# Performance work log

Hardware: AMD Instinct MI355X
Metric: run time of the kernel (lower is better)

Reference implementation:

```python
import jax, jax.numpy as jnp
import numpy as np

L, B, S, D, H, FF = 6, 6, 7, 512, 8, 2048  # layers, support-set size+1, nodes(1 verb + 6 nouns), dim, heads, ffn
HD = D // H


def setup_inputs() -> dict:
    key = jax.random.key(0)
    ks = jax.random.split(key, 16)
    n = lambda k, shape: jax.random.normal(k, shape, dtype=jnp.float32) * 0.02
    z = lambda shape: jnp.zeros(shape, jnp.float32)
    o = lambda shape: jnp.ones(shape, jnp.float32)
    return {
        'features': jax.random.normal(ks[0], (B, S, D), dtype=jnp.float32),
        'role_tokens': jax.random.normal(ks[1], (B, S - 1, D), dtype=jnp.float32),
        'in_w': n(ks[2], (L, 3 * D, D)), 'in_b': z((L, 3 * D)),
        'out_w': n(ks[3], (L, D, D)), 'out_b': z((L, D)),
        'ln1_w': o((L, D)), 'ln1_b': z((L, D)),
        'ln2_w': o((L, D)), 'ln2_b': z((L, D)),
        'ln3_w': o((L, D)), 'ln3_b': z((L, D)),
        'ln4_w': o((L, D)), 'ln4_b': z((L, D)),
        'f1_w1': n(ks[4], (L, FF, D)), 'f1_b1': z((L, FF)),
        'f1_w2': n(ks[5], (L, D, FF)), 'f1_b2': z((L, D)),
        'f2_w1': n(ks[6], (L, FF, D)), 'f2_b1': z((L, FF)),
        'f2_w2': n(ks[7], (L, D, FF)), 'f2_b2': z((L, D)),
        'a1_w': n(ks[8], (L, D, D * 5)), 'a1_b': z((L, D)),
        'a2_w': n(ks[9], (L, D, D * 6)), 'a2_b': z((L, D)),
    }


def _ln(x, w, b):
    mu = jnp.mean(x, -1, keepdims=True)
    var = jnp.mean(jnp.square(x - mu), -1, keepdims=True)
    return (x - mu) * jax.lax.rsqrt(var + 1e-5) * w + b


def _forward(features, role_tokens, in_w, in_b, out_w, out_b, ln1_w, ln1_b, ln2_w, ln2_b,
             ln3_w, ln3_b, ln4_w, ln4_b, f1_w1, f1_b1, f1_w2, f1_b2, f2_w1, f2_b1,
             f2_w2, f2_b2, a1_w, a1_b, a2_w, a2_b):
    def step(x, p):
        (iw, ib, ow, ob, l1w, l1b, l2w, l2b, l3w, l3b, l4w, l4b,
         w11, b11, w12, b12, w21, b21, w22, b22, aw1, ab1, aw2, ab2) = p
        # batched tiny self-attention over the 7 nodes of each of the 6 support examples
        src = x.at[:, 1:, :].add(role_tokens)                      # role embed on noun slots only
        qkv = jnp.einsum('bsd,ed->bse', src, iw) + ib              # (B,S,3D)
        q, k, v = jnp.split(qkv, 3, axis=-1)
        q = q.reshape(B, S, H, HD); k = k.reshape(B, S, H, HD); v = v.reshape(B, S, H, HD)
        att = jax.nn.softmax(jnp.einsum('bqhd,bkhd->bhqk', q, k) / jnp.sqrt(jnp.float32(HD)), axis=-1)
        ctx = jnp.einsum('bhqk,bkhd->bqhd', att, v).reshape(B, S, D)
        msg = jnp.einsum('bsd,ed->bse', ctx, ow) + ob              # (B,S,D)
        verb_msg = msg[:, 0, :]                                    # (B,D)
        noun_msg = msg[:, 1:, :]                                   # (B,S-1,D)
        # gated concat-aggregation
        agg_verb = jax.nn.sigmoid(verb_msg[1:].reshape(-1) @ aw1.T + ab1)  # (D,) from 5 support verb msgs
        agg_noun = jax.nn.sigmoid(noun_msg[0].reshape(-1) @ aw2.T + ab2)   # (D,) from 6 target noun msgs
        # noun update for target example (index 0)
        s = _ln(x[0, 1:, :] + agg_verb, l1w, l1b)                  # (6,D)
        s = _ln(s + (jax.nn.relu(s @ w11.T + b11) @ w12.T + b12), l2w, l2b)
        # verb update for target example
        t = _ln(x[0, 0, :] + agg_noun, l3w, l3b)                   # (D,)
        t = _ln(t + (jax.nn.relu(t @ w21.T + b21) @ w22.T + b22), l4w, l4b)
        new_self = jnp.concatenate([t[None, :], s], axis=0)        # (S,D)
        return jnp.concatenate([new_self[None], x[1:]], axis=0), None

    params = (in_w, in_b, out_w, out_b, ln1_w, ln1_b, ln2_w, ln2_b, ln3_w, ln3_b,
              ln4_w, ln4_b, f1_w1, f1_b1, f1_w2, f1_b2, f2_w1, f2_b1, f2_w2, f2_b2,
              a1_w, a1_b, a2_w, a2_b)
    out, _ = jax.lax.scan(step, features, params)
    return out[0:1]                                                # (1,7,512)


def reference(features, role_tokens, in_w, in_b, out_w, out_b, ln1_w, ln1_b, ln2_w, ln2_b,
              ln3_w, ln3_b, ln4_w, ln4_b, f1_w1, f1_b1, f1_w2, f1_b2, f2_w1, f2_b1,
              f2_w2, f2_b2, a1_w, a1_b, a2_w, a2_b):
    return _forward(features, role_tokens, in_w, in_b, out_w, out_b, ln1_w, ln1_b,
                    ln2_w, ln2_b, ln3_w, ln3_b, ln4_w, ln4_b, f1_w1, f1_b1, f1_w2, f1_b2,
                    f2_w1, f2_b1, f2_w2, f2_b2, a1_w, a1_b, a2_w, a2_b)
```

## Files before the change

kernel.cpp:

```cpp
#include <hip/hip_runtime.h>
#include <math.h>

#define NL 6
#define NB 6
#define NS 7
#define ND 512
#define NH 8
#define HDIM 64
#define NFF 2048
#define NROWS (NB*NS)

__device__ __forceinline__ float wave_sum(float v) {
    v += __shfl_down(v, 32, 64);
    v += __shfl_down(v, 16, 64);
    v += __shfl_down(v, 8, 64);
    v += __shfl_down(v, 4, 64);
    v += __shfl_down(v, 2, 64);
    v += __shfl_down(v, 1, 64);
    return v;
}

__device__ __forceinline__ float dot512(const float* __restrict__ a,
                                        const float* __restrict__ b, int lane) {
    int d0 = lane * 8;
    float4 a1 = *(const float4*)(a + d0);
    float4 a2 = *(const float4*)(a + d0 + 4);
    float4 b1 = *(const float4*)(b + d0);
    float4 b2 = *(const float4*)(b + d0 + 4);
    return a1.x*b1.x + a1.y*b1.y + a1.z*b1.z + a1.w*b1.w
         + a2.x*b2.x + a2.y*b2.y + a2.z*b2.z + a2.w*b2.w;
}

__global__ void qkv_kernel(const float* __restrict__ features,
                           const float* __restrict__ role,
                           const float* __restrict__ cur,
                           const float* __restrict__ iw,
                           const float* __restrict__ ib,
                           float* __restrict__ qkv) {
    int gw = (blockIdx.x * blockDim.x + threadIdx.x) >> 6;
    int lane = threadIdx.x & 63;
    if (gw >= NROWS * 1536) return;
    int row = gw / 1536;
    int e = gw - row * 1536;
    int b = row / NS, s = row - b * NS;
    const float* src = (b == 0) ? (cur + s * ND) : (features + row * ND);
    int d0 = lane * 8;
    float4 s1 = *(const float4*)(src + d0);
    float4 s2 = *(const float4*)(src + d0 + 4);
    if (s > 0) {
        const float* rp = role + (b * (NS-1) + (s-1)) * ND + d0;
        float4 r1 = *(const float4*)(rp);
        float4 r2 = *(const float4*)(rp + 4);
        s1.x += r1.x; s1.y += r1.y; s1.z += r1.z; s1.w += r1.w;
        s2.x += r2.x; s2.y += r2.y; s2.z += r2.z; s2.w += r2.w;
    }
    const float* wr = iw + e * ND + d0;
    float4 w1 = *(const float4*)(wr);
    float4 w2 = *(const float4*)(wr + 4);
    float acc = s1.x*w1.x + s1.y*w1.y + s1.z*w1.z + s1.w*w1.w
              + s2.x*w2.x + s2.y*w2.y + s2.z*w2.z + s2.w*w2.w;
    acc = wave_sum(acc);
    if (lane == 0) qkv[row * 1536 + e] = acc + ib[e];
}

__global__ void attn_kernel(const float* __restrict__ qkv, float* __restrict__ ctx) {
    int b = blockIdx.x >> 3, h = blockIdx.x & 7;
    int lane = threadIdx.x;
    __shared__ float q[NS][HDIM], k[NS][HDIM], v[NS][HDIM], att[NS][NS];
    for (int s = 0; s < NS; s++) {
        const float* base = qkv + (size_t)(b*NS + s) * 1536 + h * HDIM + lane;
        q[s][lane] = base[0];
        k[s][lane] = base[ND];
        v[s][lane] = base[2*ND];
    }
    __syncthreads();
    if (lane < NS*NS) {
        int i = lane / NS, j = lane - (lane / NS) * NS;
        float acc = 0.f;
        for (int d = 0; d < HDIM; d++) acc += q[i][d] * k[j][d];
        att[i][j] = acc * 0.125f;
    }
    __syncthreads();
    if (lane < NS) {
        float m = -1e30f;
        for (int j = 0; j < NS; j++) m = fmaxf(m, att[lane][j]);
        float e[NS]; float sum = 0.f;
        for (int j = 0; j < NS; j++) { e[j] = expf(att[lane][j] - m); sum += e[j]; }
        float inv = 1.f / sum;
        for (int j = 0; j < NS; j++) att[lane][j] = e[j] * inv;
    }
    __syncthreads();
    for (int s = 0; s < NS; s++) {
        float acc = 0.f;
        for (int j = 0; j < NS; j++) acc += att[s][j] * v[j][lane];
        ctx[(size_t)(b*NS + s) * ND + h * HDIM + lane] = acc;
    }
}

__global__ void msg_kernel(const float* __restrict__ ctx,
                           const float* __restrict__ ow,
                           const float* __restrict__ ob,
                           float* __restrict__ msg) {
    int gw = (blockIdx.x * blockDim.x + threadIdx.x) >> 6;
    int lane = threadIdx.x & 63;
    if (gw >= NROWS * ND) return;
    int row = gw / ND, e = gw - row * ND;
    float acc = wave_sum(dot512(ctx + (size_t)row * ND, ow + (size_t)e * ND, lane));
    if (lane == 0) msg[row * ND + e] = acc + ob[e];
}

__global__ void agg_kernel(const float* __restrict__ msg,
                           const float* __restrict__ aw1, const float* __restrict__ ab1,
                           const float* __restrict__ aw2, const float* __restrict__ ab2,
                           float* __restrict__ aggv, float* __restrict__ aggn) {
    int gw = (blockIdx.x * blockDim.x + threadIdx.x) >> 6;
    int lane = threadIdx.x & 63;
    if (gw < ND) {
        int j = gw;
        float acc = 0.f;
        for (int c = 0; c < 5; c++)
            acc += dot512(msg + (size_t)(c+1)*NS*ND, aw1 + (size_t)j*2560 + c*ND, lane);
        acc = wave_sum(acc);
        if (lane == 0) aggv[j] = 1.f / (1.f + expf(-(acc + ab1[j])));
    } else if (gw < 2*ND) {
        int j = gw - ND;
        float acc = 0.f;
        for (int c = 0; c < 6; c++)
            acc += dot512(msg + (size_t)(c+1)*ND, aw2 + (size_t)j*3072 + c*ND, lane);
        acc = wave_sum(acc);
        if (lane == 0) aggn[j] = 1.f / (1.f + expf(-(acc + ab2[j])));
    }
}

__global__ void ln13_kernel(const float* __restrict__ cur,
                            const float* __restrict__ aggv, const float* __restrict__ aggn,
                            const float* __restrict__ l1w, const float* __restrict__ l1b,
                            const float* __restrict__ l3w, const float* __restrict__ l3b,
                            float* __restrict__ xln) {
    int r = blockIdx.x, t = threadIdx.x;
    const float* agg = (r == 0) ? aggn : aggv;
    const float* w   = (r == 0) ? l3w : l1w;
    const float* bb  = (r == 0) ? l3b : l1b;
    float x0 = cur[r*ND + t]       + agg[t];
    float x1 = cur[r*ND + 256 + t] + agg[256 + t];
    __shared__ float sd[4];
    int lane = t & 63, wv = t >> 6;
    float v = wave_sum(x0 + x1);
    if (lane == 0) sd[wv] = v;
    __syncthreads();
    float mu = (sd[0] + sd[1] + sd[2] + sd[3]) * (1.f / ND);
    __syncthreads();
    float d0 = x0 - mu, d1 = x1 - mu;
    v = wave_sum(d0*d0 + d1*d1);
    if (lane == 0) sd[wv] = v;
    __syncthreads();
    float var = (sd[0] + sd[1] + sd[2] + sd[3]) * (1.f / ND);
    float inv = rsqrtf(var + 1e-5f);
    xln[r*ND + t]       = d0 * inv * w[t]     + bb[t];
    xln[r*ND + 256 + t] = d1 * inv * w[256+t] + bb[256+t];
}

__global__ void ffa_kernel(const float* __restrict__ xln,
                           const float* __restrict__ w11, const float* __restrict__ b11,
                           const float* __restrict__ w21, const float* __restrict__ b21,
                           float* __restrict__ h) {
    int gw = (blockIdx.x * blockDim.x + threadIdx.x) >> 6;
    int lane = threadIdx.x & 63;
    if (gw >= NS * NFF) return;
    int r = gw / NFF, f = gw - r * NFF;
    const float* W = (r == 0) ? (w21 + (size_t)f * ND) : (w11 + (size_t)f * ND);
    const float* bias = (r == 0) ? b21 : b11;
    float acc = wave_sum(dot512(xln + r * ND, W, lane));
    if (lane == 0) h[r * NFF + f] = fmaxf(acc + bias[f], 0.f);
}

__global__ void ffb_kernel(const float* __restrict__ xln, const float* __restrict__ hbuf,
                           const float* __restrict__ w12, const float* __restrict__ b12,
                           const float* __restrict__ w22, const float* __restrict__ b22,
                           float* __restrict__ ff) {
    int gw = (blockIdx.x * blockDim.x + threadIdx.x) >> 6;
    int lane = threadIdx.x & 63;
    if (gw >= NS * ND) return;
    int r = gw / ND, d = gw - r * ND;
    const float* W = (r == 0) ? (w22 + (size_t)d * NFF) : (w12 + (size_t)d * NFF);
    const float* bias = (r == 0) ? b22 : b12;
    const float* hin = hbuf + r * NFF;
    float acc = 0.f;
    for (int c = 0; c < 4; c++) acc += dot512(hin + c*ND, W + c*ND, lane);
    acc = wave_sum(acc);
    if (lane == 0) ff[r * ND + d] = xln[r * ND + d] + acc + bias[d];
}

__global__ void ln24_kernel(const float* __restrict__ ff,
                            const float* __restrict__ l2w, const float* __restrict__ l2b,
                            const float* __restrict__ l4w, const float* __restrict__ l4b,
                            float* __restrict__ cur, float* __restrict__ outp) {
    int r = blockIdx.x, t = threadIdx.x;
    const float* w  = (r == 0) ? l4w : l2w;
    const float* bb = (r == 0) ? l4b : l2b;
    float x0 = ff[r*ND + t], x1 = ff[r*ND + 256 + t];
    __shared__ float sd[4];
    int lane = t & 63, wv = t >> 6;
    float v = wave_sum(x0 + x1);
    if (lane == 0) sd[wv] = v;
    __syncthreads();
    float mu = (sd[0] + sd[1] + sd[2] + sd[3]) * (1.f / ND);
    __syncthreads();
    float d0 = x0 - mu, d1 = x1 - mu;
    v = wave_sum(d0*d0 + d1*d1);
    if (lane == 0) sd[wv] = v;
    __syncthreads();
    float var = (sd[0] + sd[1] + sd[2] + sd[3]) * (1.f / ND);
    float inv = rsqrtf(var + 1e-5f);
    float y0 = d0 * inv * w[t]     + bb[t];
    float y1 = d1 * inv * w[256+t] + bb[256+t];
    cur[r*ND + t]       = y0;
    cur[r*ND + 256 + t] = y1;
    if (outp) {
        outp[r*ND + t]       = y0;
        outp[r*ND + 256 + t] = y1;
    }
}

extern "C" void kernel_launch(void* const* d_in, const int* in_sizes, int n_in,
                              void* d_out, int out_size, void* d_ws, size_t ws_size,
                              hipStream_t stream) {
    const float* features = (const float*)d_in[0];
    const float* role     = (const float*)d_in[1];
    const float* in_w  = (const float*)d_in[2];
    const float* in_b  = (const float*)d_in[3];
    const float* out_w = (const float*)d_in[4];
    const float* out_b = (const float*)d_in[5];
    const float* ln1_w = (const float*)d_in[6];
    const float* ln1_b = (const float*)d_in[7];
    const float* ln2_w = (const float*)d_in[8];
    const float* ln2_b = (const float*)d_in[9];
    const float* ln3_w = (const float*)d_in[10];
    const float* ln3_b = (const float*)d_in[11];
    const float* ln4_w = (const float*)d_in[12];
    const float* ln4_b = (const float*)d_in[13];
    const float* f1_w1 = (const float*)d_in[14];
    const float* f1_b1 = (const float*)d_in[15];
    const float* f1_w2 = (const float*)d_in[16];
    const float* f1_b2 = (const float*)d_in[17];
    const float* f2_w1 = (const float*)d_in[18];
    const float* f2_b1 = (const float*)d_in[19];
    const float* f2_w2 = (const float*)d_in[20];
    const float* f2_b2 = (const float*)d_in[21];
    const float* a1_w  = (const float*)d_in[22];
    const float* a1_b  = (const float*)d_in[23];
    const float* a2_w  = (const float*)d_in[24];
    const float* a2_b  = (const float*)d_in[25];

    float* ws   = (float*)d_ws;
    float* cur  = ws;
    float* qkv  = ws + 3584;
    float* ctx  = qkv + 64512;
    float* msg  = ctx + 21504;
    float* aggv = msg + 21504;
    float* aggn = aggv + 512;
    float* xln  = aggn + 512;
    float* hbuf = xln + 3584;
    float* ff   = hbuf + 14336;

    hipMemcpyAsync(cur, features, 3584 * sizeof(float), hipMemcpyDeviceToDevice, stream);

    for (int l = 0; l < NL; l++) {
        qkv_kernel<<<NROWS*1536/4, 256, 0, stream>>>(
            features, role, cur, in_w + (size_t)l*1536*ND, in_b + (size_t)l*1536, qkv);
        attn_kernel<<<NB*NH, 64, 0, stream>>>(qkv, ctx);
        msg_kernel<<<NROWS*ND/4, 256, 0, stream>>>(
            ctx, out_w + (size_t)l*ND*ND, out_b + (size_t)l*ND, msg);
        agg_kernel<<<2*ND/4, 256, 0, stream>>>(
            msg, a1_w + (size_t)l*ND*2560, a1_b + (size_t)l*ND,
                 a2_w + (size_t)l*ND*3072, a2_b + (size_t)l*ND, aggv, aggn);
        ln13_kernel<<<NS, 256, 0, stream>>>(
            cur, aggv, aggn, ln1_w + (size_t)l*ND, ln1_b + (size_t)l*ND,
            ln3_w + (size_t)l*ND, ln3_b + (size_t)l*ND, xln);
        ffa_kernel<<<NS*NFF/4, 256, 0, stream>>>(
            xln, f1_w1 + (size_t)l*NFF*ND, f1_b1 + (size_t)l*NFF,
                 f2_w1 + (size_t)l*NFF*ND, f2_b1 + (size_t)l*NFF, hbuf);
        ffb_kernel<<<NS*ND/4, 256, 0, stream>>>(
            xln, hbuf, f1_w2 + (size_t)l*ND*NFF, f1_b2 + (size_t)l*ND,
                       f2_w2 + (size_t)l*ND*NFF, f2_b2 + (size_t)l*ND, ff);
        ln24_kernel<<<NS, 256, 0, stream>>>(
            ff, ln2_w + (size_t)l*ND, ln2_b + (size_t)l*ND,
                ln4_w + (size_t)l*ND, ln4_b + (size_t)l*ND,
            cur, (l == NL-1) ? (float*)d_out : nullptr);
    }
}
```

Measured before the change: 474.8 us.

## Replace per-layer kernel chain with single persistent kernel and grid barriers

Replaces the eight kernels launched per layer with one persistent 256-block kernel that uses software grid barriers built on atomics. Because only example 0 depends on the previous layer, the support-example K/V projections, their attention, out-projection and aggregation are precomputed for all layers up front. The serial per-layer path then handles only the target example. The change also fuses the layer norms into neighbouring stages and reuses register-held weights across several rows. It removes launch overhead and redundant per-layer work, at the cost of relying on all blocks being co-resident for the spin barriers and of extra workspace.

```diff
diff --git a/kernel.cpp b/kernel.cpp
--- a/kernel.cpp
+++ b/kernel.cpp
@@ -2,13 +2,8 @@
 #include <math.h>
 
 #define NL 6
-#define NB 6
-#define NS 7
 #define ND 512
-#define NH 8
-#define HDIM 64
 #define NFF 2048
-#define NROWS (NB*NS)
 
 __device__ __forceinline__ float wave_sum(float v) {
     v += __shfl_down(v, 32, 64);
@@ -19,9 +14,25 @@
     v += __shfl_down(v, 1, 64);
     return v;
 }
-
-__device__ __forceinline__ float dot512(const float* __restrict__ a,
-                                        const float* __restrict__ b, int lane) {
+__device__ __forceinline__ float wave_sum_all(float v) {
+    v += __shfl_xor(v, 32, 64);
+    v += __shfl_xor(v, 16, 64);
+    v += __shfl_xor(v, 8, 64);
+    v += __shfl_xor(v, 4, 64);
+    v += __shfl_xor(v, 2, 64);
+    v += __shfl_xor(v, 1, 64);
+    return v;
+}
+
+__device__ __forceinline__ float dot8(const float* a, int lane, float4 w1, float4 w2) {
+    int d0 = lane * 8;
+    float4 x1 = *(const float4*)(a + d0);
+    float4 x2 = *(const float4*)(a + d0 + 4);
+    return x1.x*w1.x + x1.y*w1.y + x1.z*w1.z + x1.w*w1.w
+         + x2.x*w2.x + x2.y*w2.y + x2.z*w2.z + x2.w*w2.w;
+}
+__device__ __forceinline__ float dotg(const float* __restrict__ a,
+                                      const float* __restrict__ b, int lane) {
     int d0 = lane * 8;
     float4 a1 = *(const float4*)(a + d0);
     float4 a2 = *(const float4*)(a + d0 + 4);
@@ -31,194 +42,366 @@
          + a2.x*b2.x + a2.y*b2.y + a2.z*b2.z + a2.w*b2.w;
 }
 
-__global__ void qkv_kernel(const float* __restrict__ features,
-                           const float* __restrict__ role,
-                           const float* __restrict__ cur,
-                           const float* __restrict__ iw,
-                           const float* __restrict__ ib,
-                           float* __restrict__ qkv) {
-    int gw = (blockIdx.x * blockDim.x + threadIdx.x) >> 6;
-    int lane = threadIdx.x & 63;
-    if (gw >= NROWS * 1536) return;
-    int row = gw / 1536;
-    int e = gw - row * 1536;
-    int b = row / NS, s = row - b * NS;
-    const float* src = (b == 0) ? (cur + s * ND) : (features + row * ND);
-    int d0 = lane * 8;
-    float4 s1 = *(const float4*)(src + d0);
-    float4 s2 = *(const float4*)(src + d0 + 4);
-    if (s > 0) {
-        const float* rp = role + (b * (NS-1) + (s-1)) * ND + d0;
-        float4 r1 = *(const float4*)(rp);
-        float4 r2 = *(const float4*)(rp + 4);
-        s1.x += r1.x; s1.y += r1.y; s1.z += r1.z; s1.w += r1.w;
-        s2.x += r2.x; s2.y += r2.y; s2.z += r2.z; s2.w += r2.w;
-    }
-    const float* wr = iw + e * ND + d0;
-    float4 w1 = *(const float4*)(wr);
-    float4 w2 = *(const float4*)(wr + 4);
-    float acc = s1.x*w1.x + s1.y*w1.y + s1.z*w1.z + s1.w*w1.w
-              + s2.x*w2.x + s2.y*w2.y + s2.z*w2.z + s2.w*w2.w;
-    acc = wave_sum(acc);
-    if (lane == 0) qkv[row * 1536 + e] = acc + ib[e];
-}
-
-__global__ void attn_kernel(const float* __restrict__ qkv, float* __restrict__ ctx) {
-    int b = blockIdx.x >> 3, h = blockIdx.x & 7;
-    int lane = threadIdx.x;
-    __shared__ float q[NS][HDIM], k[NS][HDIM], v[NS][HDIM], att[NS][NS];
-    for (int s = 0; s < NS; s++) {
-        const float* base = qkv + (size_t)(b*NS + s) * 1536 + h * HDIM + lane;
-        q[s][lane] = base[0];
-        k[s][lane] = base[ND];
-        v[s][lane] = base[2*ND];
-    }
+__device__ __forceinline__ void stats8(float4 f1, float4 f2, float& mu, float& inv) {
+    float s = f1.x+f1.y+f1.z+f1.w + f2.x+f2.y+f2.z+f2.w;
+    s = wave_sum_all(s);
+    mu = s * (1.f/512.f);
+    float q = (f1.x-mu)*(f1.x-mu) + (f1.y-mu)*(f1.y-mu) + (f1.z-mu)*(f1.z-mu) + (f1.w-mu)*(f1.w-mu)
+            + (f2.x-mu)*(f2.x-mu) + (f2.y-mu)*(f2.y-mu) + (f2.z-mu)*(f2.z-mu) + (f2.w-mu)*(f2.w-mu);
+    q = wave_sum_all(q);
+    inv = rsqrtf(q * (1.f/512.f) + 1e-5f);
+}
+__device__ __forceinline__ void ln_apply(float4& f1, float4& f2, float mu, float inv,
+                                         const float* __restrict__ w,
+                                         const float* __restrict__ b, int d0) {
+    float4 w1 = *(const float4*)(w + d0), w2 = *(const float4*)(w + d0 + 4);
+    float4 b1 = *(const float4*)(b + d0), b2 = *(const float4*)(b + d0 + 4);
+    f1.x = (f1.x-mu)*inv*w1.x + b1.x; f1.y = (f1.y-mu)*inv*w1.y + b1.y;
+    f1.z = (f1.z-mu)*inv*w1.z + b1.z; f1.w = (f1.w-mu)*inv*w1.w + b1.w;
+    f2.x = (f2.x-mu)*inv*w2.x + b2.x; f2.y = (f2.y-mu)*inv*w2.y + b2.y;
+    f2.z = (f2.z-mu)*inv*w2.z + b2.z; f2.w = (f2.w-mu)*inv*w2.w + b2.w;
+}
+
+__device__ __forceinline__ void gbar(unsigned* bar, int k) {
+    __threadfence();
     __syncthreads();
-    if (lane < NS*NS) {
-        int i = lane / NS, j = lane - (lane / NS) * NS;
-        float acc = 0.f;
-        for (int d = 0; d < HDIM; d++) acc += q[i][d] * k[j][d];
-        att[i][j] = acc * 0.125f;
+    if (threadIdx.x == 0) {
+        int sub = blockIdx.x & 7;
+        unsigned v = __hip_atomic_fetch_add(&bar[sub*16], 1u, __ATOMIC_RELAXED, __HIP_MEMORY_SCOPE_AGENT);
+        if (v == 32u*(unsigned)(k+1) - 1u) {
+            unsigned tt = __hip_atomic_fetch_add(&bar[128], 1u, __ATOMIC_RELAXED, __HIP_MEMORY_SCOPE_AGENT);
+            if (tt == 8u*(unsigned)(k+1) - 1u)
+                __hip_atomic_fetch_add(&bar[144], 1u, __ATOMIC_RELEASE, __HIP_MEMORY_SCOPE_AGENT);
+        }
+        while (__hip_atomic_load(&bar[144], __ATOMIC_RELAXED, __HIP_MEMORY_SCOPE_AGENT) < (unsigned)(k+1))
+            __builtin_amdgcn_s_sleep(4);
     }
     __syncthreads();
-    if (lane < NS) {
-        float m = -1e30f;
-        for (int j = 0; j < NS; j++) m = fmaxf(m, att[lane][j]);
-        float e[NS]; float sum = 0.f;
-        for (int j = 0; j < NS; j++) { e[j] = expf(att[lane][j] - m); sum += e[j]; }
-        float inv = 1.f / sum;
-        for (int j = 0; j < NS; j++) att[lane][j] = e[j] * inv;
+    __threadfence();
+}
+
+__global__ __launch_bounds__(256, 2)
+void fused_persistent(const float* __restrict__ features, const float* __restrict__ role,
+                      const float* __restrict__ in_w,  const float* __restrict__ in_b,
+                      const float* __restrict__ out_w, const float* __restrict__ out_b,
+                      const float* __restrict__ ln1_w, const float* __restrict__ ln1_b,
+                      const float* __restrict__ ln2_w, const float* __restrict__ ln2_b,
+                      const float* __restrict__ ln3_w, const float* __restrict__ ln3_b,
+                      const float* __restrict__ ln4_w, const float* __restrict__ ln4_b,
+                      const float* __restrict__ f1_w1, const float* __restrict__ f1_b1,
+                      const float* __restrict__ f1_w2, const float* __restrict__ f1_b2,
+                      const float* __restrict__ f2_w1, const float* __restrict__ f2_b1,
+                      const float* __restrict__ f2_w2, const float* __restrict__ f2_b2,
+                      const float* __restrict__ a1_w,  const float* __restrict__ a1_b,
+                      const float* __restrict__ a2_w,  const float* __restrict__ a2_b,
+                      unsigned* bar, float* wsf, float* __restrict__ outp)
+{
+    __shared__ float lds[18432];
+    __shared__ float sred[16];
+    const int t = threadIdx.x, bid = blockIdx.x;
+    const int wv = t >> 6, lane = t & 63;
+    const int gw = bid * 4 + wv;
+    const int d0 = lane * 8;
+    int bk = 0;
+
+    float* qkv_pre  = wsf;
+    float* msg_pre  = qkv_pre + 322560;
+    float* aggv_pre = msg_pre + 15360;
+    float* qkv0     = aggv_pre + 3072;
+    float* msg0     = qkv0 + 10752;
+    float* aggn     = msg0 + 3072;
+    float* hbuf     = aggn + 512;
+    float* xlnws    = hbuf + 14336;
+    float* ffA      = xlnws + 3584;
+    float* ffB      = ffA + 3584;
+
+    for (int i = t; i < 35*ND; i += 256) {
+        int m = i >> 9, d = i & 511;
+        int b = m / 7 + 1, s = m - (m/7)*7;
+        float v = features[(b*7+s)*ND + d];
+        if (s > 0) v += role[(b*6 + s-1)*ND + d];
+        lds[i] = v;
     }
     __syncthreads();
-    for (int s = 0; s < NS; s++) {
-        float acc = 0.f;
-        for (int j = 0; j < NS; j++) acc += att[s][j] * v[j][lane];
-        ctx[(size_t)(b*NS + s) * ND + h * HDIM + lane] = acc;
-    }
-}
-
-__global__ void msg_kernel(const float* __restrict__ ctx,
-                           const float* __restrict__ ow,
-                           const float* __restrict__ ob,
-                           float* __restrict__ msg) {
-    int gw = (blockIdx.x * blockDim.x + threadIdx.x) >> 6;
-    int lane = threadIdx.x & 63;
-    if (gw >= NROWS * ND) return;
-    int row = gw / ND, e = gw - row * ND;
-    float acc = wave_sum(dot512(ctx + (size_t)row * ND, ow + (size_t)e * ND, lane));
-    if (lane == 0) msg[row * ND + e] = acc + ob[e];
-}
-
-__global__ void agg_kernel(const float* __restrict__ msg,
-                           const float* __restrict__ aw1, const float* __restrict__ ab1,
-                           const float* __restrict__ aw2, const float* __restrict__ ab2,
-                           float* __restrict__ aggv, float* __restrict__ aggn) {
-    int gw = (blockIdx.x * blockDim.x + threadIdx.x) >> 6;
-    int lane = threadIdx.x & 63;
-    if (gw < ND) {
-        int j = gw;
-        float acc = 0.f;
+    for (int k = 0; k < 9; k++) {
+        int p = gw + (k << 10);
+        int l, e; bool kv;
+        if (p < 6144) { l = p >> 10; e = 512 + (p & 1023); kv = true; }
+        else { int q = p - 6144; l = q >> 9; e = q & 511; kv = false; }
+        const float* wr = in_w + ((size_t)l*1536 + e)*ND + d0;
+        float4 w1 = *(const float4*)wr, w2 = *(const float4*)(wr + 4);
+        float bias = in_b[l*1536 + e];
+        if (kv) {
+            for (int m = 0; m < 35; m++) {
+                float a = dot8(&lds[m*ND], lane, w1, w2);
+                a = wave_sum(a);
+                if (lane == 0) qkv_pre[((size_t)l*35 + m)*1536 + e] = a + bias;
+            }
+        } else {
+            for (int bb = 0; bb < 5; bb++) {
+                int m = bb * 7;
+                float a = dot8(&lds[m*ND], lane, w1, w2);
+                a = wave_sum(a);
+                if (lane == 0) qkv_pre[((size_t)l*35 + m)*1536 + e] = a + bias;
+            }
+        }
+    }
+    gbar(bar, bk++);
+
+    if (bid < 240) {
+        int g = bid >> 3, sub = bid & 7;
+        int l = g / 5, b = g - l*5 + 1;
+        float* kl = lds;
+        float* vl = lds + 3584;
+        float* ql = lds + 7168;
+        float* cl = lds + 7680;
+        float* at = lds + 8192;
+        size_t base = ((size_t)l*35 + (b-1)*7) * 1536;
+        for (int i = t; i < 3584; i += 256) {
+            int s = i >> 9, d = i & 511;
+            kl[i] = qkv_pre[base + (size_t)s*1536 + 512 + d];
+            vl[i] = qkv_pre[base + (size_t)s*1536 + 1024 + d];
+        }
+        for (int i = t; i < 512; i += 256) ql[i] = qkv_pre[base + i];
+        __syncthreads();
+        if (t < 56) {
+            int h = t / 7, kk = t - (t/7)*7;
+            float a = 0.f;
+            for (int d = 0; d < 64; d++) a += ql[h*64 + d] * kl[kk*512 + h*64 + d];
+            at[t] = a * 0.125f;
+        }
+        __syncthreads();
+        if (t < 8) {
+            float m = -1e30f;
+            for (int j = 0; j < 7; j++) m = fmaxf(m, at[t*7 + j]);
+            float e[7], ss = 0.f;
+            for (int j = 0; j < 7; j++) { e[j] = expf(at[t*7 + j] - m); ss += e[j]; }
+            float inv = 1.f / ss;
+            for (int j = 0; j < 7; j++) at[t*7 + j] = e[j] * inv;
+        }
+        __syncthreads();
+        for (int i = t; i < 512; i += 256) {
+            int h = i >> 6;
+            float a = 0.f;
+            for (int kk = 0; kk < 7; kk++) a += at[h*7 + kk] * vl[kk*512 + i];
+            cl[i] = a;
+        }
+        __syncthreads();
+        for (int i = 0; i < 16; i++) {
+            int e = sub*64 + wv*16 + i;
+            const float* wr = out_w + ((size_t)l*512 + e)*ND + d0;
+            float4 w1 = *(const float4*)wr, w2 = *(const float4*)(wr + 4);
+            float a = dot8(cl, lane, w1, w2);
+            a = wave_sum(a);
+            if (lane == 0) msg_pre[((size_t)l*5 + b-1)*512 + e] = a + out_b[l*512 + e];
+        }
+    }
+    gbar(bar, bk++);
+
+    for (int k = 0; k < 3; k++) {
+        int p = gw + (k << 10);
+        int l = p >> 9, j = p & 511;
+        const float* wj = a1_w + (size_t)l*1310720 + (size_t)j*2560;
+        float a = 0.f;
         for (int c = 0; c < 5; c++)
-            acc += dot512(msg + (size_t)(c+1)*NS*ND, aw1 + (size_t)j*2560 + c*ND, lane);
-        acc = wave_sum(acc);
-        if (lane == 0) aggv[j] = 1.f / (1.f + expf(-(acc + ab1[j])));
-    } else if (gw < 2*ND) {
-        int j = gw - ND;
-        float acc = 0.f;
-        for (int c = 0; c < 6; c++)
-            acc += dot512(msg + (size_t)(c+1)*ND, aw2 + (size_t)j*3072 + c*ND, lane);
-        acc = wave_sum(acc);
-        if (lane == 0) aggn[j] = 1.f / (1.f + expf(-(acc + ab2[j])));
-    }
-}
-
-__global__ void ln13_kernel(const float* __restrict__ cur,
-                            const float* __restrict__ aggv, const float* __restrict__ aggn,
-                            const float* __restrict__ l1w, const float* __restrict__ l1b,
-                            const float* __restrict__ l3w, const float* __restrict__ l3b,
-                            float* __restrict__ xln) {
-    int r = blockIdx.x, t = threadIdx.x;
-    const float* agg = (r == 0) ? aggn : aggv;
-    const float* w   = (r == 0) ? l3w : l1w;
-    const float* bb  = (r == 0) ? l3b : l1b;
-    float x0 = cur[r*ND + t]       + agg[t];
-    float x1 = cur[r*ND + 256 + t] + agg[256 + t];
-    __shared__ float sd[4];
-    int lane = t & 63, wv = t >> 6;
-    float v = wave_sum(x0 + x1);
-    if (lane == 0) sd[wv] = v;
-    __syncthreads();
-    float mu = (sd[0] + sd[1] + sd[2] + sd[3]) * (1.f / ND);
-    __syncthreads();
-    float d0 = x0 - mu, d1 = x1 - mu;
-    v = wave_sum(d0*d0 + d1*d1);
-    if (lane == 0) sd[wv] = v;
-    __syncthreads();
-    float var = (sd[0] + sd[1] + sd[2] + sd[3]) * (1.f / ND);
-    float inv = rsqrtf(var + 1e-5f);
-    xln[r*ND + t]       = d0 * inv * w[t]     + bb[t];
-    xln[r*ND + 256 + t] = d1 * inv * w[256+t] + bb[256+t];
-}
-
-__global__ void ffa_kernel(const float* __restrict__ xln,
-                           const float* __restrict__ w11, const float* __restrict__ b11,
-                           const float* __restrict__ w21, const float* __restrict__ b21,
-                           float* __restrict__ h) {
-    int gw = (blockIdx.x * blockDim.x + threadIdx.x) >> 6;
-    int lane = threadIdx.x & 63;
-    if (gw >= NS * NFF) return;
-    int r = gw / NFF, f = gw - r * NFF;
-    const float* W = (r == 0) ? (w21 + (size_t)f * ND) : (w11 + (size_t)f * ND);
-    const float* bias = (r == 0) ? b21 : b11;
-    float acc = wave_sum(dot512(xln + r * ND, W, lane));
-    if (lane == 0) h[r * NFF + f] = fmaxf(acc + bias[f], 0.f);
-}
-
-__global__ void ffb_kernel(const float* __restrict__ xln, const float* __restrict__ hbuf,
-                           const float* __restrict__ w12, const float* __restrict__ b12,
-                           const float* __restrict__ w22, const float* __restrict__ b22,
-                           float* __restrict__ ff) {
-    int gw = (blockIdx.x * blockDim.x + threadIdx.x) >> 6;
-    int lane = threadIdx.x & 63;
-    if (gw >= NS * ND) return;
-    int r = gw / ND, d = gw - r * ND;
-    const float* W = (r == 0) ? (w22 + (size_t)d * NFF) : (w12 + (size_t)d * NFF);
-    const float* bias = (r == 0) ? b22 : b12;
-    const float* hin = hbuf + r * NFF;
-    float acc = 0.f;
-    for (int c = 0; c < 4; c++) acc += dot512(hin + c*ND, W + c*ND, lane);
-    acc = wave_sum(acc);
-    if (lane == 0) ff[r * ND + d] = xln[r * ND + d] + acc + bias[d];
-}
-
-__global__ void ln24_kernel(const float* __restrict__ ff,
-                            const float* __restrict__ l2w, const float* __restrict__ l2b,
-                            const float* __restrict__ l4w, const float* __restrict__ l4b,
-                            float* __restrict__ cur, float* __restrict__ outp) {
-    int r = blockIdx.x, t = threadIdx.x;
-    const float* w  = (r == 0) ? l4w : l2w;
-    const float* bb = (r == 0) ? l4b : l2b;
-    float x0 = ff[r*ND + t], x1 = ff[r*ND + 256 + t];
-    __shared__ float sd[4];
-    int lane = t & 63, wv = t >> 6;
-    float v = wave_sum(x0 + x1);
-    if (lane == 0) sd[wv] = v;
-    __syncthreads();
-    float mu = (sd[0] + sd[1] + sd[2] + sd[3]) * (1.f / ND);
-    __syncthreads();
-    float d0 = x0 - mu, d1 = x1 - mu;
-    v = wave_sum(d0*d0 + d1*d1);
-    if (lane == 0) sd[wv] = v;
-    __syncthreads();
-    float var = (sd[0] + sd[1] + sd[2] + sd[3]) * (1.f / ND);
-    float inv = rsqrtf(var + 1e-5f);
-    float y0 = d0 * inv * w[t]     + bb[t];
-    float y1 = d1 * inv * w[256+t] + bb[256+t];
-    cur[r*ND + t]       = y0;
-    cur[r*ND + 256 + t] = y1;
-    if (outp) {
-        outp[r*ND + t]       = y0;
-        outp[r*ND + 256 + t] = y1;
+            a += dotg(msg_pre + ((size_t)l*5 + c)*512, wj + c*512, lane);
+        a = wave_sum(a);
+        if (lane == 0) aggv_pre[l*512 + j] = 1.f / (1.f + expf(-(a + a1_b[l*512 + j])));
+    }
+    gbar(bar, bk++);
+
+    const float* ffprev = nullptr;
+    #pragma unroll 1
+    for (int l = 0; l < NL; l++) {
+        float* ffcur = (l & 1) ? ffB : ffA;
+
+        for (int rr = wv; rr < 7; rr += 4) {
+            float4 f1, f2;
+            if (l == 0) {
+                const float* sp = features + rr*ND + d0;
+                f1 = *(const float4*)sp; f2 = *(const float4*)(sp + 4);
+            } else {
+                const float* sp = ffprev + rr*ND + d0;
+                f1 = *(const float4*)sp; f2 = *(const float4*)(sp + 4);
+                float mu, inv; stats8(f1, f2, mu, inv);
+                const float* w  = ((rr == 0) ? ln4_w : ln2_w) + (size_t)(l-1)*ND;
+                const float* bb = ((rr == 0) ? ln4_b : ln2_b) + (size_t)(l-1)*ND;
+                ln_apply(f1, f2, mu, inv, w, bb, d0);
+            }
+            if (rr > 0) {
+                const float* rp = role + (size_t)(rr-1)*ND + d0;
+                float4 r1 = *(const float4*)rp, r2 = *(const float4*)(rp + 4);
+                f1.x += r1.x; f1.y += r1.y; f1.z += r1.z; f1.w += r1.w;
+                f2.x += r2.x; f2.y += r2.y; f2.z += r2.z; f2.w += r2.w;
+            }
+            *(float4*)&lds[rr*ND + d0] = f1;
+            *(float4*)&lds[rr*ND + d0 + 4] = f2;
+        }
+        __syncthreads();
+        for (int e = gw; e < 1536; e += 1024) {
+            const float* wr = in_w + ((size_t)l*1536 + e)*ND + d0;
+            float4 w1 = *(const float4*)wr, w2 = *(const float4*)(wr + 4);
+            float bias = in_b[l*1536 + e];
+            for (int s = 0; s < 7; s++) {
+                float a = dot8(&lds[s*ND], lane, w1, w2);
+                a = wave_sum(a);
+                if (lane == 0) qkv0[s*1536 + e] = a + bias;
+            }
+        }
+        gbar(bar, bk++);
+
+        {
+            float* kl = lds;
+            float* vl = lds + 3584;
+            float* ql = lds + 7168;
+            float* cl = lds + 10240;
+            float* at = lds + 13312;
+            for (int i = t; i < 3584; i += 256) {
+                int s = i >> 9, d = i & 511;
+                kl[i] = qkv0[s*1536 + 512 + d];
+                vl[i] = qkv0[s*1536 + 1024 + d];
+            }
+            for (int i = t; i < 3072; i += 256) {
+                int s = (i >> 9) + 1;
+                ql[i] = qkv0[s*1536 + (i & 511)];
+            }
+            __syncthreads();
+            for (int idx = t; idx < 336; idx += 256) {
+                int qr = idx / 56, rem = idx - qr*56;
+                int h = rem / 7, kk = rem - (rem/7)*7;
+                float a = 0.f;
+                for (int d = 0; d < 64; d++) a += ql[qr*512 + h*64 + d] * kl[kk*512 + h*64 + d];
+                at[idx] = a * 0.125f;
+            }
+            __syncthreads();
+            if (t < 48) {
+                int qr = t >> 3, h = t & 7;
+                float* ap = at + qr*56 + h*7;
+                float m = -1e30f;
+                for (int j = 0; j < 7; j++) m = fmaxf(m, ap[j]);
+                float e[7], ss = 0.f;
+                for (int j = 0; j < 7; j++) { e[j] = expf(ap[j] - m); ss += e[j]; }
+                float inv = 1.f / ss;
+                for (int j = 0; j < 7; j++) ap[j] = e[j] * inv;
+            }
+            __syncthreads();
+            for (int i = t; i < 3072; i += 256) {
+                int qr = i >> 9, d = i & 511, h = d >> 6;
+                const float* ap = at + qr*56 + h*7;
+                float a = 0.f;
+                for (int kk = 0; kk < 7; kk++) a += ap[kk] * vl[kk*512 + d];
+                cl[i] = a;
+            }
+            __syncthreads();
+            for (int i = 0; i < 3; i++) {
+                int o = bid*12 + wv*3 + i;
+                int s = (o >> 9) + 1, e = o & 511;
+                const float* wr = out_w + ((size_t)l*512 + e)*ND + d0;
+                float4 w1 = *(const float4*)wr, w2 = *(const float4*)(wr + 4);
+                float a = dot8(&cl[(s-1)*512], lane, w1, w2);
+                a = wave_sum(a);
+                if (lane == 0) msg0[(s-1)*512 + e] = a + out_b[l*512 + e];
+            }
+        }
+        gbar(bar, bk++);
+
+        {
+            int j = bid*2 + (wv >> 1), half = wv & 1;
+            const float* wj = a2_w + (size_t)l*1572864 + (size_t)j*3072 + half*1536;
+            float a = 0.f;
+            for (int c = 0; c < 3; c++)
+                a += dotg(msg0 + (half*3 + c)*512, wj + c*512, lane);
+            a = wave_sum(a);
+            if (lane == 0) sred[wv] = a;
+        }
+        __syncthreads();
+        if (t == 0) {
+            int j0 = bid*2;
+            aggn[j0]     = 1.f / (1.f + expf(-(sred[0] + sred[1] + a2_b[l*512 + j0])));
+            aggn[j0 + 1] = 1.f / (1.f + expf(-(sred[2] + sred[3] + a2_b[l*512 + j0 + 1])));
+        }
+        gbar(bar, bk++);
+
+        for (int rr = wv; rr < 7; rr += 4) {
+            float4 f1, f2;
+            if (l == 0) {
+                const float* sp = features + rr*ND + d0;
+                f1 = *(const float4*)sp; f2 = *(const float4*)(sp + 4);
+            } else {
+                const float* sp = ffprev + rr*ND + d0;
+                f1 = *(const float4*)sp; f2 = *(const float4*)(sp + 4);
+                float mu, inv; stats8(f1, f2, mu, inv);
+                const float* w  = ((rr == 0) ? ln4_w : ln2_w) + (size_t)(l-1)*ND;
+                const float* bb = ((rr == 0) ? ln4_b : ln2_b) + (size_t)(l-1)*ND;
+                ln_apply(f1, f2, mu, inv, w, bb, d0);
+            }
+            const float* ag = (rr == 0) ? aggn : (aggv_pre + l*512);
+            float4 g1 = *(const float4*)(ag + d0), g2 = *(const float4*)(ag + d0 + 4);
+            f1.x += g1.x; f1.y += g1.y; f1.z += g1.z; f1.w += g1.w;
+            f2.x += g2.x; f2.y += g2.y; f2.z += g2.z; f2.w += g2.w;
+            float mu, inv; stats8(f1, f2, mu, inv);
+            const float* w  = ((rr == 0) ? ln3_w : ln1_w) + (size_t)l*ND;
+            const float* bb = ((rr == 0) ? ln3_b : ln1_b) + (size_t)l*ND;
+            ln_apply(f1, f2, mu, inv, w, bb, d0);
+            *(float4*)&lds[rr*ND + d0] = f1;
+            *(float4*)&lds[rr*ND + d0 + 4] = f2;
+        }
+        __syncthreads();
+        if (bid == 0) for (int i = t; i < 3584; i += 256) xlnws[i] = lds[i];
+        for (int i = 0; i < 2; i++) {
+            int f = bid*8 + wv*2 + i;
+            const float* wr1 = f1_w1 + ((size_t)l*2048 + f)*ND + d0;
+            float4 p1 = *(const float4*)wr1, p2 = *(const float4*)(wr1 + 4);
+            const float* wr2 = f2_w1 + ((size_t)l*2048 + f)*ND + d0;
+            float4 q1 = *(const float4*)wr2, q2 = *(const float4*)(wr2 + 4);
+            float a = dot8(&lds[0], lane, q1, q2);
+            a = wave_sum(a);
+            if (lane == 0) hbuf[f] = fmaxf(a + f2_b1[l*2048 + f], 0.f);
+            for (int r = 1; r < 7; r++) {
+                float b = dot8(&lds[r*ND], lane, p1, p2);
+                b = wave_sum(b);
+                if (lane == 0) hbuf[r*2048 + f] = fmaxf(b + f1_b1[l*2048 + f], 0.f);
+            }
+        }
+        gbar(bar, bk++);
+
+        {
+            int d = bid*2 + (wv >> 1);
+            int rs = (wv & 1) ? 4 : 0, re = (wv & 1) ? 7 : 4;
+            for (int r = rs; r < re; r++) {
+                const float* W = ((r == 0) ? f2_w2 : f1_w2) + (size_t)l*1048576 + (size_t)d*2048;
+                float a = 0.f;
+                for (int c = 0; c < 4; c++)
+                    a += dotg(hbuf + r*2048 + c*512, W + c*512, lane);
+                a = wave_sum(a);
+                if (lane == 0) {
+                    float bias = (r == 0) ? f2_b2[l*512 + d] : f1_b2[l*512 + d];
+                    ffcur[r*512 + d] = xlnws[r*512 + d] + a + bias;
+                }
+            }
+        }
+        ffprev = ffcur;
+        gbar(bar, bk++);
+    }
+
+    if (bid < 7) {
+        int r = bid;
+        float x0 = ffprev[r*ND + t], x1 = ffprev[r*ND + 256 + t];
+        float v = wave_sum(x0 + x1);
+        if (lane == 0) sred[wv] = v;
+        __syncthreads();
+        float mu = (sred[0] + sred[1] + sred[2] + sred[3]) * (1.f/512.f);
+        __syncthreads();
+        float e0 = x0 - mu, e1 = x1 - mu;
+        v = wave_sum(e0*e0 + e1*e1);
+        if (lane == 0) sred[wv] = v;
+        __syncthreads();
+        float var = (sred[0] + sred[1] + sred[2] + sred[3]) * (1.f/512.f);
+        float inv = rsqrtf(var + 1e-5f);
+        const float* w  = ((r == 0) ? ln4_w : ln2_w) + (size_t)(NL-1)*ND;
+        const float* bb = ((r == 0) ? ln4_b : ln2_b) + (size_t)(NL-1)*ND;
+        outp[r*ND + t]       = e0*inv*w[t]       + bb[t];
+        outp[r*ND + 256 + t] = e1*inv*w[256 + t] + bb[256 + t];
     }
 }
 
@@ -252,40 +435,14 @@
     const float* a2_w  = (const float*)d_in[24];
     const float* a2_b  = (const float*)d_in[25];
 
-    float* ws   = (float*)d_ws;
-    float* cur  = ws;
-    float* qkv  = ws + 3584;
-    float* ctx  = qkv + 64512;
-    float* msg  = ctx + 21504;
-    float* aggv = msg + 21504;
-    float* aggn = aggv + 512;
-    float* xln  = aggn + 512;
-    float* hbuf = xln + 3584;
-    float* ff   = hbuf + 14336;
-
-    hipMemcpyAsync(cur, features, 3584 * sizeof(float), hipMemcpyDeviceToDevice, stream);
-
-    for (int l = 0; l < NL; l++) {
-        qkv_kernel<<<NROWS*1536/4, 256, 0, stream>>>(
-            features, role, cur, in_w + (size_t)l*1536*ND, in_b + (size_t)l*1536, qkv);
-        attn_kernel<<<NB*NH, 64, 0, stream>>>(qkv, ctx);
-        msg_kernel<<<NROWS*ND/4, 256, 0, stream>>>(
-            ctx, out_w + (size_t)l*ND*ND, out_b + (size_t)l*ND, msg);
-        agg_kernel<<<2*ND/4, 256, 0, stream>>>(
-            msg, a1_w + (size_t)l*ND*2560, a1_b + (size_t)l*ND,
-                 a2_w + (size_t)l*ND*3072, a2_b + (size_t)l*ND, aggv, aggn);
-        ln13_kernel<<<NS, 256, 0, stream>>>(
-            cur, aggv, aggn, ln1_w + (size_t)l*ND, ln1_b + (size_t)l*ND,
-            ln3_w + (size_t)l*ND, ln3_b + (size_t)l*ND, xln);
-        ffa_kernel<<<NS*NFF/4, 256, 0, stream>>>(
-            xln, f1_w1 + (size_t)l*NFF*ND, f1_b1 + (size_t)l*NFF,
-                 f2_w1 + (size_t)l*NFF*ND, f2_b1 + (size_t)l*NFF, hbuf);
-        ffb_kernel<<<NS*ND/4, 256, 0, stream>>>(
-            xln, hbuf, f1_w2 + (size_t)l*ND*NFF, f1_b2 + (size_t)l*ND,
-                       f2_w2 + (size_t)l*ND*NFF, f2_b2 + (size_t)l*ND, ff);
-        ln24_kernel<<<NS, 256, 0, stream>>>(
-            ff, ln2_w + (size_t)l*ND, ln2_b + (size_t)l*ND,
-                ln4_w + (size_t)l*ND, ln4_b + (size_t)l*ND,
-            cur, (l == NL-1) ? (float*)d_out : nullptr);
-    }
-}
+    hipMemsetAsync(d_ws, 0, 1024, stream);
+    unsigned* bar = (unsigned*)d_ws;
+    float* wsf = (float*)d_ws + 256;
+
+    fused_persistent<<<256, 256, 0, stream>>>(
+        features, role, in_w, in_b, out_w, out_b,
+        ln1_w, ln1_b, ln2_w, ln2_b, ln3_w, ln3_b, ln4_w, ln4_b,
+        f1_w1, f1_b1, f1_w2, f1_b2, f2_w1, f2_b1, f2_w2, f2_b2,
+        a1_w, a1_b, a2_w, a2_b,
+        bar, wsf, (float*)d_out);
+}
```

Result: slower. 1.629 ms (+243.1%).
